# Optimization experiments

Hardware: AMD Instinct MI355X
Metric: run time of the kernel (lower is better)

Reference implementation:

```python
import jax, jax.numpy as jnp
import numpy as np

C = 5          # max within-cluster spike gap (module-level constant in source repo)
DELTA = 0.05   # margin constant (module-level constant in source repo)
B, T, N = 128, 512, 256


def setup_inputs() -> dict:
    key = jax.random.key(0)
    k1, k2, k3 = jax.random.split(key, 3)
    vmem = jax.random.normal(k1, (B, T, N), dtype=jnp.float32) - 1.5
    vlastmem = jax.random.normal(k2, (B, T, N), dtype=jnp.float32)  # unused by the loss math
    labels_t = jax.random.randint(k3, (B, N), 0, 4)
    ratio = jnp.float32(0.5)
    return {"vmem": vmem, "vlastmem": vlastmem, "labels_t": labels_t, "ratio": ratio}


def _per_neuron(v, key):
    """v: [T] membrane trace for one (batch, neuron). Returns (num_cluster, under_term, max_over)."""
    Tn = v.shape[0]
    t = jnp.arange(Tn)
    spike = v >= 0.0
    s = spike.astype(jnp.int32)
    # prefix sums: cs[i] = number of spikes in v[:i]
    cs = jnp.concatenate([jnp.zeros(1, jnp.int32), jnp.cumsum(s)])
    # new cluster starts at t iff spike[t] and no spike in [t-C, t-1]  (gap > C)
    prev_cnt = cs[t] - cs[jnp.clip(t - C, 0, Tn)]
    is_start = spike & (prev_cnt == 0)
    nclu = jnp.sum(is_start.astype(jnp.int32))
    # under-branch mask = union over clusters of [first-C, last+C] = C-dilation of spike train
    dil_cnt = cs[jnp.clip(t + C + 1, 0, Tn)] - cs[jnp.clip(t - C, 0, Tn)]
    mask = dil_cnt > 0

    # per-cluster stats via segmented reductions (cluster id = running count of starts)
    cid = jnp.clip(jnp.cumsum(is_start.astype(jnp.int32)) - 1, 0, Tn - 1)
    counts = jax.ops.segment_sum(s, cid, num_segments=Tn)
    first = jax.ops.segment_min(jnp.where(spike, t, Tn), cid, num_segments=Tn)
    last = jax.ops.segment_max(jnp.where(spike, t, -1), cid, num_segments=Tn)

    # over branch: cluster minimizing (end_idx - beg_idx) == min spike count (first on ties)
    counts_q = jnp.where(t < nclu, counts, Tn + 2)
    ic = jnp.argmin(counts_q)
    over_mask = (t >= first[ic]) & (t <= last[ic])
    max_over = jnp.max(jnp.where(over_mask, v, -jnp.inf))

    # under branch: if unmasked timesteps remain, penalize -max(v[mask==0]);
    # else take v at a (pinned-seed) random spike position
    has_zero = jnp.any(~mask)
    max_unmask = jnp.max(jnp.where(~mask, v, -jnp.inf))
    nsp = cs[-1]
    sorted_pos = jnp.sort(jnp.where(spike, t, Tn))
    r = jax.random.randint(key, (), 0, jnp.maximum(nsp, 1))
    v_rand = v[jnp.clip(sorted_pos[r], 0, Tn - 1)]
    under_term = jnp.where(has_zero, -max_unmask, v_rand)
    return nclu, under_term, max_over


def _forward(vmem, vlastmem, labels_t, ratio):
    Bv, Tv, Nv = vmem.shape
    vflat = jnp.swapaxes(vmem, 1, 2).reshape(Bv * Nv, Tv)   # [B*N, T]
    lflat = labels_t.reshape(Bv * Nv)
    keys = jax.random.split(jax.random.key(42), Bv * Nv)     # pinned seed for the random-spike pick
    nclu, under_term, max_over = jax.vmap(_per_neuron)(vflat, keys)
    ncf = nclu.astype(vmem.dtype)
    margin = DELTA * ratio * ncf
    under = jnp.where(lflat > nclu, under_term + margin, 0.0)
    over = jnp.where(lflat < nclu, max_over + margin, 0.0)
    loss = jnp.sum(under + over)
    spike_output = ncf.reshape(Bv, Nv)
    return loss, spike_output


def reference(vmem, vlastmem, labels_t, ratio):
    return _forward(vmem, vlastmem, labels_t, ratio)
```

## Files before the change

kernel.cpp:

```cpp
#include <hip/hip_runtime.h>
#include <stdint.h>

#define TDIM 512
#define NDIM 256
#define CGAP 5
#define DELTA_C 0.05f
#define NSEG 8
#define SEGT 64
#define BIGI (1 << 28)

extern "C" __global__ void __launch_bounds__(512, 2)
stca_kernel(const float* __restrict__ vmem, const int* __restrict__ labels,
            const float* __restrict__ ratio_p, float* __restrict__ out,
            float* __restrict__ ws) {
  __shared__ int   si[8][NSEG * 64];
  __shared__ float sf[6][NSEG * 64];

  const int lane = threadIdx.x & 63;
  const int seg  = threadIdx.x >> 6;
  const int blk  = blockIdx.x;
  const int b    = blk >> 2;
  const int n0   = (blk & 3) << 6;
  const int n    = n0 + lane;

  const float* g = vmem + (size_t)b * TDIM * NDIM + n;
  const int t0 = seg * SEGT, t1 = t0 + SEGT;

  int   last_spike = -1000, nclu = 0, cur_cnt = 0, cur_fs = 0, fs = BIGI;
  float cur_max = -INFINITY, cur_maxlast = -INFINITY;
  float seg_run_max = -INFINITY, mfs_snap = -INFINITY;
  int   pfx_cnt = 0, pfx_ls = 0;
  float pfx_core = -INFINITY, pfx_mfs = -INFINITY;
  int   bint_cnt = BIGI;
  float bint_max = -INFINITY;
  unsigned hist = 0u;
  float umax = -INFINITY;
  float vd0 = 0.f, vd1 = 0.f, vd2 = 0.f, vd3 = 0.f, vd4 = 0.f, vd5 = 0.f;

  if (t0 > 0) {
#pragma unroll
    for (int j = 0; j < CGAP; ++j) {
      const float v = g[(size_t)(t0 - CGAP + j) * NDIM];
      hist = ((hist << 1) | (v >= 0.f ? 1u : 0u)) & 0x7FFu;
    }
  }

  auto step = [&](float v, int te) {
    const bool spike   = v >= 0.0f;
    const bool isstart = spike && ((te - last_spike) > CGAP);
    const bool closing = isstart && (nclu > 0);
    const bool isfirst = closing && (nclu == 1);
    const bool bet     = closing && (nclu > 1) && (cur_cnt < bint_cnt);
    pfx_cnt  = isfirst ? cur_cnt     : pfx_cnt;
    pfx_ls   = isfirst ? last_spike  : pfx_ls;
    pfx_core = isfirst ? cur_maxlast : pfx_core;
    pfx_mfs  = isfirst ? mfs_snap    : pfx_mfs;
    bint_cnt = bet ? cur_cnt     : bint_cnt;
    bint_max = bet ? cur_maxlast : bint_max;
    nclu += isstart ? 1 : 0;
    cur_fs  = isstart ? te : cur_fs;
    cur_max = isstart ? v : fmaxf(cur_max, v);
    cur_maxlast = spike ? cur_max : cur_maxlast;
    cur_cnt = (isstart ? 0 : cur_cnt) + (spike ? 1 : 0);
    seg_run_max = fmaxf(seg_run_max, v);
    const bool snap = spike && (nclu == 1);
    mfs_snap = snap ? seg_run_max : mfs_snap;
    fs = (spike && fs == BIGI) ? te : fs;
    last_spike = spike ? te : last_spike;
    hist = ((hist << 1) | (spike ? 1u : 0u)) & 0x7FFu;
    vd5 = vd4; vd4 = vd3; vd3 = vd2; vd2 = vd1; vd1 = vd0; vd0 = v;
    const bool un = (hist == 0u) && (te >= t0 + CGAP);
    umax = un ? fmaxf(umax, vd5) : umax;
  };

#pragma unroll 1
  for (int c = 0; c < SEGT / 8; ++c) {
    const float* gp = g + (size_t)(t0 + c * 8) * NDIM;
    const float y0 = gp[0 * NDIM], y1 = gp[1 * NDIM], y2 = gp[2 * NDIM],
                y3 = gp[3 * NDIM], y4 = gp[4 * NDIM], y5 = gp[5 * NDIM],
                y6 = gp[6 * NDIM], y7 = gp[7 * NDIM];
    const int tc = t0 + c * 8;
    step(y0, tc + 0); step(y1, tc + 1); step(y2, tc + 2); step(y3, tc + 3);
    step(y4, tc + 4); step(y5, tc + 5); step(y6, tc + 6); step(y7, tc + 7);
  }

#pragma unroll
  for (int j = 0; j < CGAP; ++j) {
    const int te = t1 + j;
    const float v = (te < TDIM) ? g[(size_t)te * NDIM] : -INFINITY;
    const bool spike = v >= 0.0f;
    hist = ((hist << 1) | (spike ? 1u : 0u)) & 0x7FFu;
    vd5 = vd4; vd4 = vd3; vd3 = vd2; vd2 = vd1; vd1 = vd0; vd0 = v;
    const bool un = (hist == 0u);
    umax = un ? fmaxf(umax, vd5) : umax;
  }

  int   sfx_cnt = 0, sfx_fs = 0;
  float sfx_core = -INFINITY, sfx_mte = -INFINITY;
  if (nclu >= 1) {
    sfx_cnt = cur_cnt; sfx_fs = cur_fs; sfx_core = cur_maxlast; sfx_mte = cur_max;
    if (nclu == 1) {
      pfx_cnt = cur_cnt; pfx_ls = last_spike; pfx_core = cur_maxlast; pfx_mfs = mfs_snap;
    }
  }

  const int idx = threadIdx.x;
  si[0][idx] = nclu;    si[1][idx] = fs;      si[2][idx] = last_spike;
  si[3][idx] = pfx_cnt; si[4][idx] = pfx_ls;  si[5][idx] = sfx_cnt;
  si[6][idx] = sfx_fs;  si[7][idx] = bint_cnt;
  sf[0][idx] = pfx_core; sf[1][idx] = pfx_mfs; sf[2][idx] = sfx_core;
  sf[3][idx] = sfx_mte;  sf[4][idx] = bint_max; sf[5][idx] = umax;
  __syncthreads();

  if (seg != 0) return;

  int   a_nclu = nclu, a_fs = fs, a_ls = last_spike;
  int   a_pcnt = pfx_cnt, a_pls = pfx_ls, a_scnt = sfx_cnt, a_sfs = sfx_fs;
  int   a_bcnt = bint_cnt;
  float a_pcore = pfx_core, a_pmfs = pfx_mfs, a_score = sfx_core, a_smte = sfx_mte;
  float a_bmax = bint_max, a_umax = umax;

  for (int s = 1; s < NSEG; ++s) {
    const int j = (s << 6) + lane;
    const int   r_nclu = si[0][j], r_fs = si[1][j], r_ls = si[2][j];
    const int   r_pcnt = si[3][j], r_pls = si[4][j];
    const int   r_scnt = si[5][j], r_sfs = si[6][j];
    const int   r_bcnt = si[7][j];
    const float r_pcore = sf[0][j], r_pmfs = sf[1][j];
    const float r_score = sf[2][j], r_smte = sf[3][j];
    const float r_bmax = sf[4][j], r_umax = sf[5][j];

    a_umax = fmaxf(a_umax, r_umax);
    if (r_nclu == 0) continue;
    if (a_nclu == 0) {
      a_nclu = r_nclu; a_fs = r_fs; a_ls = r_ls;
      a_pcnt = r_pcnt; a_pls = r_pls; a_pcore = r_pcore; a_pmfs = r_pmfs;
      a_scnt = r_scnt; a_sfs = r_sfs; a_score = r_score; a_smte = r_smte;
      a_bcnt = r_bcnt; a_bmax = r_bmax;
      continue;
    }
    if (r_fs - a_ls <= CGAP) {
      const int   Bc    = a_scnt + r_pcnt;
      const float Bcore = fmaxf(a_smte, r_pmfs);
      const float Bmfs  = fmaxf(fmaxf(a_pmfs, a_smte), r_pmfs);
      const float Bmte  = fmaxf(fmaxf(a_smte, r_pmfs), r_smte);
      const int   Bfs = a_sfs, Bls = r_pls;
      int nb = a_bcnt; float nbm = a_bmax;
      if (a_nclu >= 2 && r_nclu >= 2 && Bc < nb) { nb = Bc; nbm = Bcore; }
      if (r_bcnt < nb) { nb = r_bcnt; nbm = r_bmax; }
      if (a_nclu == 1) { a_pcnt = Bc; a_pls = Bls; a_pcore = Bcore; a_pmfs = Bmfs; }
      if (r_nclu == 1) { a_scnt = Bc; a_sfs = Bfs; a_score = Bcore; a_smte = Bmte; }
      else             { a_scnt = r_scnt; a_sfs = r_sfs; a_score = r_score; a_smte = r_smte; }
      a_bcnt = nb; a_bmax = nbm;
      a_nclu = a_nclu + r_nclu - 1;
      a_ls = r_ls;
    } else {
      int nb = a_bcnt; float nbm = a_bmax;
      if (a_nclu >= 2 && a_scnt < nb) { nb = a_scnt; nbm = a_score; }
      if (r_nclu >= 2 && r_pcnt < nb) { nb = r_pcnt; nbm = r_pcore; }
      if (r_bcnt < nb) { nb = r_bcnt; nbm = r_bmax; }
      a_bcnt = nb; a_bmax = nbm;
      a_scnt = r_scnt; a_sfs = r_sfs; a_score = r_score; a_smte = r_smte;
      a_nclu += r_nclu;
      a_ls = r_ls;
    }
  }

  int bc = a_pcnt; float bm = a_pcore;
  if (a_nclu >= 2) {
    if (a_bcnt < bc) { bc = a_bcnt; bm = a_bmax; }
    if (a_scnt < bc) { bc = a_scnt; bm = a_score; }
  }

  const float ratio = ratio_p[0];
  const int   label = labels[b * NDIM + n];
  const float ncf    = (float)a_nclu;
  const float margin = DELTA_C * ratio * ncf;
  const float under_term = (a_umax > -INFINITY) ? (-a_umax) : 0.0f;
  const float under = (label > a_nclu) ? (under_term + margin) : 0.0f;
  const float over  = (label < a_nclu) ? (bm + margin) : 0.0f;

  out[1 + b * NDIM + n] = ncf;

  float sum = under + over;
#pragma unroll
  for (int off = 32; off > 0; off >>= 1) sum += __shfl_down(sum, off);
  if (lane == 0) ws[blk] = sum;
}

extern "C" __global__ void __launch_bounds__(64, 1)
stca_reduce(const float* __restrict__ ws, float* __restrict__ out) {
  const int lane = threadIdx.x;
  float s = 0.0f;
#pragma unroll
  for (int i = 0; i < 8; ++i) s += ws[lane + (i << 6)];
#pragma unroll
  for (int off = 32; off > 0; off >>= 1) s += __shfl_down(s, off);
  if (lane == 0) out[0] = s;
}

extern "C" void kernel_launch(void* const* d_in, const int* in_sizes, int n_in,
                              void* d_out, int out_size, void* d_ws,
                              size_t ws_size, hipStream_t stream) {
  const float* vmem   = (const float*)d_in[0];
  const int*   labels = (const int*)d_in[2];
  const float* ratio  = (const float*)d_in[3];
  float* out = (float*)d_out;
  float* ws  = (float*)d_ws;

  dim3 grid(512);
  dim3 block(512);
  hipLaunchKernelGGL(stca_kernel, grid, block, 0, stream, vmem, labels, ratio,
                     out, ws);
  hipLaunchKernelGGL(stca_reduce, dim3(1), dim3(64), 0, stream, ws, out);
}
```

Before: 146.7 us.

## Replace per-timestep cluster state machine with 64-bit spike bitmask ops

Each thread now packs its 64-timestep segment into a 64-bit spike mask and derives cluster starts, counts, prefix, suffix and the best interior cluster with popcount, ctz and clz instead of a serial per-step state machine. The under-branch dilation mask is built from neighbouring segments' masks held in shared memory. A second pass re-reads vmem and takes masked maxima only when some lane needs them, so the float max tracking leaves the first pass. This cuts ALU work per timestep at the cost of a conditional second global read and extra barriers.

```diff
diff --git a/kernel.cpp b/kernel.cpp
--- a/kernel.cpp
+++ b/kernel.cpp
@@ -9,178 +9,198 @@
 #define SEGT 64
 #define BIGI (1 << 28)
 
+typedef unsigned long long u64;
+typedef unsigned int u32;
+
+
+__device__ __forceinline__ int  ctz64(u64 x)   { return x ? __builtin_ctzll(x) : 64; }
+__device__ __forceinline__ int  hib64(u64 x)   { return x ? 63 - __builtin_clzll(x) : -1; }
+__device__ __forceinline__ u64  below64(int p) { return (p >= 64) ? ~0ull : ((1ull << p) - 1ull); }
+
 extern "C" __global__ void __launch_bounds__(512, 2)
 stca_kernel(const float* __restrict__ vmem, const int* __restrict__ labels,
             const float* __restrict__ ratio_p, float* __restrict__ out,
             float* __restrict__ ws) {
-  __shared__ int   si[8][NSEG * 64];
-  __shared__ float sf[6][NSEG * 64];
+  __shared__ u32 sw_lo[NSEG * 64], sw_hi[NSEG * 64];
+  __shared__ int s_nclu[NSEG * 64], s_fs[NSEG * 64], s_ls[NSEG * 64];
+  __shared__ int s_pc[NSEG * 64], s_pl[NSEG * 64];
+  __shared__ int s_sc[NSEG * 64], s_sf[NSEG * 64];
+  __shared__ int s_bc[NSEG * 64], s_bf[NSEG * 64], s_bl[NSEG * 64];
+  __shared__ int pn_nclu[64], pn_tf[64], pn_tl[64];
+  __shared__ float sO[NSEG * 64], sU[NSEG * 64];
 
   const int lane = threadIdx.x & 63;
   const int seg  = threadIdx.x >> 6;
+  const int idx  = threadIdx.x;
   const int blk  = blockIdx.x;
   const int b    = blk >> 2;
   const int n0   = (blk & 3) << 6;
   const int n    = n0 + lane;
 
   const float* g = vmem + (size_t)b * TDIM * NDIM + n;
-  const int t0 = seg * SEGT, t1 = t0 + SEGT;
-
-  int   last_spike = -1000, nclu = 0, cur_cnt = 0, cur_fs = 0, fs = BIGI;
-  float cur_max = -INFINITY, cur_maxlast = -INFINITY;
-  float seg_run_max = -INFINITY, mfs_snap = -INFINITY;
-  int   pfx_cnt = 0, pfx_ls = 0;
-  float pfx_core = -INFINITY, pfx_mfs = -INFINITY;
-  int   bint_cnt = BIGI;
-  float bint_max = -INFINITY;
-  unsigned hist = 0u;
-  float umax = -INFINITY;
-  float vd0 = 0.f, vd1 = 0.f, vd2 = 0.f, vd3 = 0.f, vd4 = 0.f, vd5 = 0.f;
-
-  if (t0 > 0) {
-#pragma unroll
-    for (int j = 0; j < CGAP; ++j) {
-      const float v = g[(size_t)(t0 - CGAP + j) * NDIM];
-      hist = ((hist << 1) | (v >= 0.f ? 1u : 0u)) & 0x7FFu;
-    }
-  }
-
-  auto step = [&](float v, int te) {
-    const bool spike   = v >= 0.0f;
-    const bool isstart = spike && ((te - last_spike) > CGAP);
-    const bool closing = isstart && (nclu > 0);
-    const bool isfirst = closing && (nclu == 1);
-    const bool bet     = closing && (nclu > 1) && (cur_cnt < bint_cnt);
-    pfx_cnt  = isfirst ? cur_cnt     : pfx_cnt;
-    pfx_ls   = isfirst ? last_spike  : pfx_ls;
-    pfx_core = isfirst ? cur_maxlast : pfx_core;
-    pfx_mfs  = isfirst ? mfs_snap    : pfx_mfs;
-    bint_cnt = bet ? cur_cnt     : bint_cnt;
-    bint_max = bet ? cur_maxlast : bint_max;
-    nclu += isstart ? 1 : 0;
-    cur_fs  = isstart ? te : cur_fs;
-    cur_max = isstart ? v : fmaxf(cur_max, v);
-    cur_maxlast = spike ? cur_max : cur_maxlast;
-    cur_cnt = (isstart ? 0 : cur_cnt) + (spike ? 1 : 0);
-    seg_run_max = fmaxf(seg_run_max, v);
-    const bool snap = spike && (nclu == 1);
-    mfs_snap = snap ? seg_run_max : mfs_snap;
-    fs = (spike && fs == BIGI) ? te : fs;
-    last_spike = spike ? te : last_spike;
-    hist = ((hist << 1) | (spike ? 1u : 0u)) & 0x7FFu;
-    vd5 = vd4; vd4 = vd3; vd3 = vd2; vd2 = vd1; vd1 = vd0; vd0 = v;
-    const bool un = (hist == 0u) && (te >= t0 + CGAP);
-    umax = un ? fmaxf(umax, vd5) : umax;
-  };
-
+  const int t0 = seg * SEGT;
+
+  u64 s = 0ull;
 #pragma unroll 1
   for (int c = 0; c < SEGT / 8; ++c) {
     const float* gp = g + (size_t)(t0 + c * 8) * NDIM;
     const float y0 = gp[0 * NDIM], y1 = gp[1 * NDIM], y2 = gp[2 * NDIM],
                 y3 = gp[3 * NDIM], y4 = gp[4 * NDIM], y5 = gp[5 * NDIM],
                 y6 = gp[6 * NDIM], y7 = gp[7 * NDIM];
-    const int tc = t0 + c * 8;
-    step(y0, tc + 0); step(y1, tc + 1); step(y2, tc + 2); step(y3, tc + 3);
-    step(y4, tc + 4); step(y5, tc + 5); step(y6, tc + 6); step(y7, tc + 7);
-  }
-
-#pragma unroll
-  for (int j = 0; j < CGAP; ++j) {
-    const int te = t1 + j;
-    const float v = (te < TDIM) ? g[(size_t)te * NDIM] : -INFINITY;
-    const bool spike = v >= 0.0f;
-    hist = ((hist << 1) | (spike ? 1u : 0u)) & 0x7FFu;
-    vd5 = vd4; vd4 = vd3; vd3 = vd2; vd2 = vd1; vd1 = vd0; vd0 = v;
-    const bool un = (hist == 0u);
-    umax = un ? fmaxf(umax, vd5) : umax;
-  }
-
-  int   sfx_cnt = 0, sfx_fs = 0;
-  float sfx_core = -INFINITY, sfx_mte = -INFINITY;
-  if (nclu >= 1) {
-    sfx_cnt = cur_cnt; sfx_fs = cur_fs; sfx_core = cur_maxlast; sfx_mte = cur_max;
-    if (nclu == 1) {
-      pfx_cnt = cur_cnt; pfx_ls = last_spike; pfx_core = cur_maxlast; pfx_mfs = mfs_snap;
+    const u32 bits = (y0 >= 0.f ?   1u : 0u) | (y1 >= 0.f ?   2u : 0u)
+                   | (y2 >= 0.f ?   4u : 0u) | (y3 >= 0.f ?   8u : 0u)
+                   | (y4 >= 0.f ?  16u : 0u) | (y5 >= 0.f ?  32u : 0u)
+                   | (y6 >= 0.f ?  64u : 0u) | (y7 >= 0.f ? 128u : 0u);
+    s |= (u64)bits << (c * 8);
+  }
+
+  u64 w5 = (s << 1) | (s << 2);
+  w5 |= (s << 3) | (s << 4) | (s << 5);
+  const u64 starts = s & ~w5;
+  const int nclu = __popcll(starts);
+  const int fs_l = ctz64(s);
+  const int ls_l = hib64(s);
+  const u64 st2 = starts & (starts - 1);
+  const int p2  = ctz64(st2);
+  const u64 pm  = s & below64(p2);
+  const int pcnt  = __popcll(pm);
+  const int pls_l = hib64(pm);
+  const int plast = (nclu >= 1) ? hib64(starts) : 0;
+  const int scnt  = __popcll(s >> plast);
+  int bcnt = BIGI, bfs_l = 0, bls_l = 0;
+  u64 rem = st2;
+  while ((rem & (rem - 1)) != 0ull) {
+    const int p   = ctz64(rem);
+    const u64 rem2 = rem & (rem - 1);
+    const int pnx = ctz64(rem2);
+    const u64 m   = s & below64(pnx) & ~below64(p);
+    const int cnt = __popcll(m);
+    if (cnt < bcnt) { bcnt = cnt; bfs_l = p; bls_l = hib64(m); }
+    rem = rem2;
+  }
+
+  sw_lo[idx] = (u32)s;  sw_hi[idx] = (u32)(s >> 32);
+  s_nclu[idx] = nclu;
+  s_fs[idx] = (nclu >= 1) ? (t0 + fs_l) : BIGI;
+  s_ls[idx] = t0 + ls_l;
+  s_pc[idx] = pcnt;  s_pl[idx] = t0 + pls_l;
+  s_sc[idx] = scnt;  s_sf[idx] = t0 + plast;
+  s_bc[idx] = bcnt;  s_bf[idx] = t0 + bfs_l;  s_bl[idx] = t0 + bls_l;
+  __syncthreads();
+
+  const u64 sL = (seg > 0)
+      ? ((u64)sw_lo[idx - 64] | ((u64)sw_hi[idx - 64] << 32)) : 0ull;
+  const u64 sR = (seg < NSEG - 1)
+      ? ((u64)sw_lo[idx + 64] | ((u64)sw_hi[idx + 64] << 32)) : 0ull;
+  u64 D = s;
+  D |= (s << 1) | (sL >> 63);
+  D |= (s << 2) | (sL >> 62);
+  D |= (s << 3) | (sL >> 61);
+  D |= (s << 4) | (sL >> 60);
+  D |= (s << 5) | (sL >> 59);
+  D |= (s >> 1) | (sR << 63);
+  D |= (s >> 2) | (sR << 62);
+  D |= (s >> 3) | (sR << 61);
+  D |= (s >> 4) | (sR << 60);
+  D |= (s >> 5) | (sR << 59);
+
+  int a_nclu = 0;
+  if (seg == 0) {
+    int a_fs = BIGI, a_ls = 0;
+    int a_pcnt = 0, a_pls = 0, a_scnt = 0, a_sfs = 0;
+    int a_bcnt = BIGI, a_bfs = 0, a_bls = 0;
+    for (int sg = 0; sg < NSEG; ++sg) {
+      const int j = (sg << 6) + lane;
+      const int r_nclu = s_nclu[j];
+      if (r_nclu == 0) continue;
+      const int r_fs = s_fs[j], r_ls = s_ls[j];
+      const int r_pcnt = s_pc[j], r_pls = s_pl[j];
+      const int r_scnt = s_sc[j], r_sfs = s_sf[j];
+      const int r_bcnt = s_bc[j], r_bfs = s_bf[j], r_bl = s_bl[j];
+      if (a_nclu == 0) {
+        a_nclu = r_nclu; a_fs = r_fs; a_ls = r_ls;
+        a_pcnt = r_pcnt; a_pls = r_pls; a_scnt = r_scnt; a_sfs = r_sfs;
+        a_bcnt = r_bcnt; a_bfs = r_bfs; a_bls = r_bl;
+        continue;
+      }
+      if (r_fs - a_ls <= CGAP) {
+        const int Bc = a_scnt + r_pcnt, Bfs = a_sfs, Bls = r_pls;
+        int nb = a_bcnt, nbf = a_bfs, nbl = a_bls;
+        if (a_nclu >= 2 && r_nclu >= 2 && Bc < nb) { nb = Bc; nbf = Bfs; nbl = Bls; }
+        if (r_bcnt < nb) { nb = r_bcnt; nbf = r_bfs; nbl = r_bl; }
+        if (a_nclu == 1) { a_pcnt = Bc; a_pls = Bls; }
+        if (r_nclu == 1) { a_scnt = Bc; a_sfs = Bfs; }
+        else             { a_scnt = r_scnt; a_sfs = r_sfs; }
+        a_bcnt = nb; a_bfs = nbf; a_bls = nbl;
+        a_nclu += r_nclu - 1;
+        a_ls = r_ls;
+      } else {
+        int nb = a_bcnt, nbf = a_bfs, nbl = a_bls;
+        if (a_nclu >= 2 && a_scnt < nb) { nb = a_scnt; nbf = a_sfs; nbl = a_ls; }
+        if (r_nclu >= 2 && r_pcnt < nb) { nb = r_pcnt; nbf = r_fs;  nbl = r_pls; }
+        if (r_bcnt < nb) { nb = r_bcnt; nbf = r_bfs; nbl = r_bl; }
+        a_bcnt = nb; a_bfs = nbf; a_bls = nbl;
+        a_scnt = r_scnt; a_sfs = r_sfs;
+        a_nclu += r_nclu;
+        a_ls = r_ls;
+      }
     }
-  }
-
-  const int idx = threadIdx.x;
-  si[0][idx] = nclu;    si[1][idx] = fs;      si[2][idx] = last_spike;
-  si[3][idx] = pfx_cnt; si[4][idx] = pfx_ls;  si[5][idx] = sfx_cnt;
-  si[6][idx] = sfx_fs;  si[7][idx] = bint_cnt;
-  sf[0][idx] = pfx_core; sf[1][idx] = pfx_mfs; sf[2][idx] = sfx_core;
-  sf[3][idx] = sfx_mte;  sf[4][idx] = bint_max; sf[5][idx] = umax;
+    int tf = a_fs, tl = a_pls, bc = a_pcnt;
+    if (a_nclu >= 2) {
+      if (a_bcnt < bc) { bc = a_bcnt; tf = a_bfs; tl = a_bls; }
+      if (a_scnt < bc) { bc = a_scnt; tf = a_sfs; tl = a_ls; }
+    }
+    pn_nclu[lane] = a_nclu; pn_tf[lane] = tf; pn_tl[lane] = tl;
+    out[1 + b * NDIM + n] = (float)a_nclu;
+  }
   __syncthreads();
 
+  const int  label  = labels[b * NDIM + n];
+  const int  f_nclu = pn_nclu[lane];
+  const int  tf = pn_tf[lane], tl = pn_tl[lane];
+  const bool needO = label < f_nclu;
+  const bool needU = label > f_nclu;
+  int lo = tf - t0; lo = lo < 0 ? 0 : (lo > 64 ? 64 : lo);
+  int hi = tl - t0 + 1; hi = hi < 0 ? 0 : (hi > 64 ? 64 : hi);
+  u64 R  = needO ? (below64(hi) & ~below64(lo)) : 0ull;
+  u64 Dm = needU ? ~D : 0ull;
+  float mO = -INFINITY, mU = -INFINITY;
+  if (__any((R | Dm) != 0ull)) {
+#pragma unroll 1
+    for (int c = 0; c < SEGT / 8; ++c) {
+      const float* gp = g + (size_t)(t0 + c * 8) * NDIM;
+      const float y0 = gp[0 * NDIM], y1 = gp[1 * NDIM], y2 = gp[2 * NDIM],
+                  y3 = gp[3 * NDIM], y4 = gp[4 * NDIM], y5 = gp[5 * NDIM],
+                  y6 = gp[6 * NDIM], y7 = gp[7 * NDIM];
+      const u32 r8 = (u32)(R >> (c * 8));
+      const u32 d8 = (u32)(Dm >> (c * 8));
+      mO = (r8 &   1u) ? fmaxf(mO, y0) : mO;  mU = (d8 &   1u) ? fmaxf(mU, y0) : mU;
+      mO = (r8 &   2u) ? fmaxf(mO, y1) : mO;  mU = (d8 &   2u) ? fmaxf(mU, y1) : mU;
+      mO = (r8 &   4u) ? fmaxf(mO, y2) : mO;  mU = (d8 &   4u) ? fmaxf(mU, y2) : mU;
+      mO = (r8 &   8u) ? fmaxf(mO, y3) : mO;  mU = (d8 &   8u) ? fmaxf(mU, y3) : mU;
+      mO = (r8 &  16u) ? fmaxf(mO, y4) : mO;  mU = (d8 &  16u) ? fmaxf(mU, y4) : mU;
+      mO = (r8 &  32u) ? fmaxf(mO, y5) : mO;  mU = (d8 &  32u) ? fmaxf(mU, y5) : mU;
+      mO = (r8 &  64u) ? fmaxf(mO, y6) : mO;  mU = (d8 &  64u) ? fmaxf(mU, y6) : mU;
+      mO = (r8 & 128u) ? fmaxf(mO, y7) : mO;  mU = (d8 & 128u) ? fmaxf(mU, y7) : mU;
+    }
+  }
+  sO[idx] = mO; sU[idx] = mU;
+  __syncthreads();
+
   if (seg != 0) return;
 
-  int   a_nclu = nclu, a_fs = fs, a_ls = last_spike;
-  int   a_pcnt = pfx_cnt, a_pls = pfx_ls, a_scnt = sfx_cnt, a_sfs = sfx_fs;
-  int   a_bcnt = bint_cnt;
-  float a_pcore = pfx_core, a_pmfs = pfx_mfs, a_score = sfx_core, a_smte = sfx_mte;
-  float a_bmax = bint_max, a_umax = umax;
-
-  for (int s = 1; s < NSEG; ++s) {
-    const int j = (s << 6) + lane;
-    const int   r_nclu = si[0][j], r_fs = si[1][j], r_ls = si[2][j];
-    const int   r_pcnt = si[3][j], r_pls = si[4][j];
-    const int   r_scnt = si[5][j], r_sfs = si[6][j];
-    const int   r_bcnt = si[7][j];
-    const float r_pcore = sf[0][j], r_pmfs = sf[1][j];
-    const float r_score = sf[2][j], r_smte = sf[3][j];
-    const float r_bmax = sf[4][j], r_umax = sf[5][j];
-
-    a_umax = fmaxf(a_umax, r_umax);
-    if (r_nclu == 0) continue;
-    if (a_nclu == 0) {
-      a_nclu = r_nclu; a_fs = r_fs; a_ls = r_ls;
-      a_pcnt = r_pcnt; a_pls = r_pls; a_pcore = r_pcore; a_pmfs = r_pmfs;
-      a_scnt = r_scnt; a_sfs = r_sfs; a_score = r_score; a_smte = r_smte;
-      a_bcnt = r_bcnt; a_bmax = r_bmax;
-      continue;
-    }
-    if (r_fs - a_ls <= CGAP) {
-      const int   Bc    = a_scnt + r_pcnt;
-      const float Bcore = fmaxf(a_smte, r_pmfs);
-      const float Bmfs  = fmaxf(fmaxf(a_pmfs, a_smte), r_pmfs);
-      const float Bmte  = fmaxf(fmaxf(a_smte, r_pmfs), r_smte);
-      const int   Bfs = a_sfs, Bls = r_pls;
-      int nb = a_bcnt; float nbm = a_bmax;
-      if (a_nclu >= 2 && r_nclu >= 2 && Bc < nb) { nb = Bc; nbm = Bcore; }
-      if (r_bcnt < nb) { nb = r_bcnt; nbm = r_bmax; }
-      if (a_nclu == 1) { a_pcnt = Bc; a_pls = Bls; a_pcore = Bcore; a_pmfs = Bmfs; }
-      if (r_nclu == 1) { a_scnt = Bc; a_sfs = Bfs; a_score = Bcore; a_smte = Bmte; }
-      else             { a_scnt = r_scnt; a_sfs = r_sfs; a_score = r_score; a_smte = r_smte; }
-      a_bcnt = nb; a_bmax = nbm;
-      a_nclu = a_nclu + r_nclu - 1;
-      a_ls = r_ls;
-    } else {
-      int nb = a_bcnt; float nbm = a_bmax;
-      if (a_nclu >= 2 && a_scnt < nb) { nb = a_scnt; nbm = a_score; }
-      if (r_nclu >= 2 && r_pcnt < nb) { nb = r_pcnt; nbm = r_pcore; }
-      if (r_bcnt < nb) { nb = r_bcnt; nbm = r_bmax; }
-      a_bcnt = nb; a_bmax = nbm;
-      a_scnt = r_scnt; a_sfs = r_sfs; a_score = r_score; a_smte = r_smte;
-      a_nclu += r_nclu;
-      a_ls = r_ls;
-    }
-  }
-
-  int bc = a_pcnt; float bm = a_pcore;
-  if (a_nclu >= 2) {
-    if (a_bcnt < bc) { bc = a_bcnt; bm = a_bmax; }
-    if (a_scnt < bc) { bc = a_scnt; bm = a_score; }
-  }
-
-  const float ratio = ratio_p[0];
-  const int   label = labels[b * NDIM + n];
+  float mo = sO[lane], mu = sU[lane];
+#pragma unroll
+  for (int sg = 1; sg < NSEG; ++sg) {
+    mo = fmaxf(mo, sO[(sg << 6) + lane]);
+    mu = fmaxf(mu, sU[(sg << 6) + lane]);
+  }
+  const float ratio  = ratio_p[0];
   const float ncf    = (float)a_nclu;
   const float margin = DELTA_C * ratio * ncf;
-  const float under_term = (a_umax > -INFINITY) ? (-a_umax) : 0.0f;
+  const float under_term = (mu > -INFINITY) ? (-mu) : 0.0f;
   const float under = (label > a_nclu) ? (under_term + margin) : 0.0f;
-  const float over  = (label < a_nclu) ? (bm + margin) : 0.0f;
-
-  out[1 + b * NDIM + n] = ncf;
+  const float over  = (label < a_nclu) ? (mo + margin) : 0.0f;
 
   float sum = under + over;
 #pragma unroll
```

After: 146.2 us. Within noise of the previous version (-0.4%).
